# Performance work log

Hardware: AMD Instinct MI355X
Metric: run time of the kernel (lower is better)

## Reference

```python
import jax, jax.numpy as jnp
import numpy as np

B, C, H, W = 64, 256, 32, 32
K, D = 1024, 256
COMMIT = 0.25
DECAY = 0.99
EPS = 1e-05


def setup_inputs() -> dict:
    key = jax.random.key(0)
    k1, k2, k3 = jax.random.split(key, 3)
    return {
        "inputs": jax.random.normal(k1, (B, C, H, W), dtype=jnp.float32),
        "embedding": jax.random.normal(k2, (K, D), dtype=jnp.float32),
        "ema_cluster_size": jnp.zeros((K,), dtype=jnp.float32),
        "ema_w": jax.random.normal(k3, (K, D), dtype=jnp.float32),
    }


def reference(inputs, embedding, ema_cluster_size, ema_w):
    # NCHW -> NHWC, flatten to [N, D]
    x = jnp.transpose(inputs, (0, 2, 3, 1))  # [B,H,W,D]
    in_shape = x.shape
    flat = x.reshape(-1, D)  # [N, D]

    dist = (jnp.sum(flat * flat, axis=1, keepdims=True)
            + jnp.sum(embedding * embedding, axis=1)
            - 2.0 * jnp.matmul(flat, embedding.T))
    idx = jnp.argmin(dist, axis=1)  # [N] int
    encodings = jax.nn.one_hot(idx, K, dtype=flat.dtype)  # [N, K]

    quantized = jnp.matmul(encodings, embedding).reshape(in_shape)  # [B,H,W,D]

    # EMA updates (training branch)
    cluster = ema_cluster_size * DECAY + (1.0 - DECAY) * jnp.sum(encodings, axis=0)
    n = jnp.sum(cluster)
    cluster = (cluster + EPS) / (n + K * EPS) * n
    dw = jnp.matmul(encodings.T, flat)  # [K, D]
    new_ema_w = ema_w * DECAY + (1.0 - DECAY) * dw
    new_embedding = new_ema_w / cluster[:, None]

    # commitment loss (quantized detached)
    e_latent_loss = jnp.mean((jax.lax.stop_gradient(quantized) - x) ** 2)
    loss = COMMIT * e_latent_loss

    # straight-through estimator
    quantized_st = x + jax.lax.stop_gradient(quantized - x)

    avg_probs = jnp.mean(encodings, axis=0)
    vq_entropy = -jnp.sum(avg_probs * jnp.log(avg_probs + 1e-10))

    out = jnp.transpose(quantized_st, (0, 3, 1, 2))  # back to NCHW
    return out, loss, vq_entropy, encodings, cluster, new_ema_w, new_embedding
```

## Files before the change

### kernel.cpp

```cpp
#include <hip/hip_runtime.h>

#define B_    64
#define C_    256
#define H_    32
#define W_    32
#define K_    1024
#define D_    256
#define HW_   1024
#define N_    65536
#define NELEM 16777216
#define DECAY_ 0.99f
#define OMD_   0.01f
#define EPS_   1e-5f
#define TAU_   0.05f

#define OFF_LOSS    16777216
#define OFF_ENT     16777217
#define OFF_ENC     16777218
#define OFF_CLUSTER 83886082
#define OFF_NEWW    83887106
#define OFF_NEWEMB  84149250

#define OFF_XHI     (OFF_ENC + 2)
#define OFF_XLO     (OFF_XHI + 8388608)
#define OFF_EHI     (OFF_XLO + 8388608)
#define OFF_ELO     (OFF_EHI + 131072)
#define OFF_SORT2   (OFF_ELO + 131072)
#define ZTAIL_ABS   33884168
#define ZTAIL_F4    12500478
#define ZHEAD_F4    4276737

typedef __attribute__((ext_vector_type(8)))  short short8;
typedef __attribute__((ext_vector_type(16))) float floatx16;

__device__ __forceinline__ unsigned short f2bf(float f) {
    unsigned u = __float_as_uint(f);
    return (unsigned short)((u + 0x7fffu + ((u >> 16) & 1u)) >> 16);
}
__device__ __forceinline__ float bf2f(unsigned short h) {
    return __uint_as_float(((unsigned)h) << 16);
}

__global__ __launch_bounds__(256) void k_zero(float* __restrict__ dw, int* __restrict__ small_) {
    int g = blockIdx.x * 256 + threadIdx.x;
    dw[g] = 0.0f;
    if (g < 1026) small_[g] = 0;
}

__global__ __launch_bounds__(64) void k_prep_e(const float* __restrict__ emb,
                                               unsigned short* __restrict__ ehi,
                                               unsigned short* __restrict__ elo,
                                               float* __restrict__ enorm) {
    const int k = blockIdx.x;
    const int t = threadIdx.x;
    float4 v = ((const float4*)(emb + (size_t)k * D_))[t];
    float s = v.x * v.x + v.y * v.y + v.z * v.z + v.w * v.w;
    ushort4 hi, lo;
    {
        float f[4] = {v.x, v.y, v.z, v.w};
        unsigned short h[4], l[4];
        #pragma unroll
        for (int j = 0; j < 4; ++j) {
            h[j] = f2bf(f[j]);
            l[j] = f2bf(f[j] - bf2f(h[j]));
        }
        hi = make_ushort4(h[0], h[1], h[2], h[3]);
        lo = make_ushort4(l[0], l[1], l[2], l[3]);
    }
    size_t o = ((size_t)(k >> 5) << 13) + ((size_t)(t >> 2) << 9)
             + (((size_t)(t >> 1) & 1) << 8) + ((size_t)(k & 31) << 3) + ((t & 1) << 2);
    *(ushort4*)(ehi + o) = hi;
    *(ushort4*)(elo + o) = lo;
    #pragma unroll
    for (int off = 32; off > 0; off >>= 1) s += __shfl_down(s, off);
    if (t == 0) enorm[k] = s;
}

__global__ __launch_bounds__(256) void k_prep_x(const float* __restrict__ inp,
                                                unsigned short* __restrict__ xhi,
                                                unsigned short* __restrict__ xlo) {
    __shared__ float tile[32][257];
    const int tid = threadIdx.x;
    const int bid = blockIdx.x;
    const int dt = bid & 7;
    const int ht = (bid >> 3) & 3;
    const int b = bid >> 5;
    const int d0 = dt * 32;
    const int hw0 = ht * 256;
    const float* src = inp + (size_t)b * (C_ * HW_) + (size_t)d0 * HW_ + hw0;
    #pragma unroll
    for (int i = 0; i < 8; ++i) {
        int idx4 = i * 256 + tid;
        int dl = idx4 >> 6;
        int nl4 = (idx4 & 63) * 4;
        float4 v = *(const float4*)(src + (size_t)dl * HW_ + nl4);
        tile[dl][nl4] = v.x; tile[dl][nl4 + 1] = v.y;
        tile[dl][nl4 + 2] = v.z; tile[dl][nl4 + 3] = v.w;
    }
    __syncthreads();
    const int nbase = b * HW_ + hw0;
    #pragma unroll
    for (int i = 0; i < 4; ++i) {
        int f8 = i * 256 + tid;
        int nl = f8 >> 2;
        int dpos = (f8 & 3) * 8;
        union { unsigned short u[8]; short8 v; } ph, pl;
        #pragma unroll
        for (int j = 0; j < 8; ++j) {
            float f = -2.0f * tile[dpos + j][nl];
            unsigned short h = f2bf(f);
            ph.u[j] = h;
            pl.u[j] = f2bf(f - bf2f(h));
        }
        size_t o = (size_t)(nbase + nl) * D_ + d0 + dpos;
        *(short8*)(xhi + o) = ph.v;
        *(short8*)(xlo + o) = pl.v;
    }
}

__device__ __forceinline__ void stage_tile(const unsigned short* __restrict__ gh,
                                           const unsigned short* __restrict__ gl,
                                           unsigned short* sh, unsigned short* sl,
                                           int tid) {
    #pragma unroll
    for (int i = 0; i < 4; ++i) {
        __builtin_amdgcn_global_load_lds(
            (const __attribute__((address_space(1))) unsigned int*)(gh + i * 2048 + tid * 8),
            (__attribute__((address_space(3))) unsigned int*)(sh + i * 2048 + tid * 8),
            16, 0, 0);
        __builtin_amdgcn_global_load_lds(
            (const __attribute__((address_space(1))) unsigned int*)(gl + i * 2048 + tid * 8),
            (__attribute__((address_space(3))) unsigned int*)(sl + i * 2048 + tid * 8),
            16, 0, 0);
    }
}

__global__ __launch_bounds__(256, 2) void k_argmin(
    const unsigned short* __restrict__ xhi, const unsigned short* __restrict__ xlo,
    const unsigned short* __restrict__ ehi, const unsigned short* __restrict__ elo,
    const float* __restrict__ enorm, int* __restrict__ idx_out,
    int* __restrict__ flagcount, int* __restrict__ flaglist,
    float4* __restrict__ encz)
{
    __shared__ unsigned short smem[2][2][8192];
    const int tid = threadIdx.x;
    const int w = tid >> 6;
    const int lane = tid & 63;
    const int c32 = lane & 31;
    const int h = lane >> 5;
    const int r0 = blockIdx.x * 128 + w * 32;
    const int gtid = blockIdx.x * 256 + tid;
    const float4 z4 = make_float4(0.f, 0.f, 0.f, 0.f);

    short8 Ahi[16], Alo[16];
    {
        const unsigned short* pa = xhi + (size_t)(r0 + c32) * D_ + h * 8;
        const unsigned short* pl = xlo + (size_t)(r0 + c32) * D_ + h * 8;
        #pragma unroll
        for (int ds = 0; ds < 16; ++ds) {
            Ahi[ds] = *(const short8*)(pa + ds * 16);
            Alo[ds] = *(const short8*)(pl + ds * 16);
        }
    }

    float b1[16], b2[16];
    int bi[16];
    #pragma unroll
    for (int i = 0; i < 16; ++i) { b1[i] = 3.0e38f; b2[i] = 3.0e38f; bi[i] = 0; }

    stage_tile(ehi, elo, &smem[0][0][0], &smem[0][1][0], tid);
    __syncthreads();

    const int rb = (h << 8) + (c32 << 3);

    int cb = 0;
    for (int ct = 0; ct < 32; ++ct) {
        if (ct + 1 < 32) {
            stage_tile(ehi + (size_t)(ct + 1) * 8192, elo + (size_t)(ct + 1) * 8192,
                       &smem[cb ^ 1][0][0], &smem[cb ^ 1][1][0], tid);
        }
        #pragma unroll
        for (int jj = 0; jj < 3; ++jj) {
            int zi = (ct * 3 + jj) * 131072 + gtid;
            if (zi < ZTAIL_F4) encz[zi] = z4;
        }
        const int col = ct * 32 + c32;
        const float en = enorm[col];
        const unsigned short* sbh = &smem[cb][0][rb];
        const unsigned short* sbl = &smem[cb][1][rb];
        floatx16 hh, cr;
        #pragma unroll
        for (int i = 0; i < 16; ++i) { hh[i] = 0.0f; cr[i] = 0.0f; }
        #pragma unroll
        for (int ds = 0; ds < 16; ++ds) {
            short8 bh = *(const short8*)(sbh + ds * 512);
            short8 bl = *(const short8*)(sbl + ds * 512);
            hh = __builtin_amdgcn_mfma_f32_32x32x16_bf16(Ahi[ds], bh, hh, 0, 0, 0);
            cr = __builtin_amdgcn_mfma_f32_32x32x16_bf16(Ahi[ds], bl, cr, 0, 0, 0);
            cr = __builtin_amdgcn_mfma_f32_32x32x16_bf16(Alo[ds], bh, cr, 0, 0, 0);
        }
        #pragma unroll
        for (int r = 0; r < 16; ++r) {
            float v = hh[r] + cr[r] + en;
            bool lt = v < b1[r];
            float nb2 = lt ? b1[r] : fminf(v, b2[r]);
            b2[r] = nb2;
            b1[r] = lt ? v : b1[r];
            bi[r] = lt ? col : bi[r];
        }
        __syncthreads();
        cb ^= 1;
    }

    #pragma unroll
    for (int r = 0; r < 16; ++r) {
        float B1 = b1[r], B2 = b2[r];
        int Bi = bi[r];
        #pragma unroll
        for (int mask = 1; mask <= 16; mask <<= 1) {
            float v1 = __shfl_xor(B1, mask);
            float v2 = __shfl_xor(B2, mask);
            int i1 = __shfl_xor(Bi, mask);
            if (v1 < B1 || (v1 == B1 && i1 < Bi)) {
                B2 = fminf(fminf(B1, B2), v2);
                B1 = v1; Bi = i1;
            } else {
                B2 = fminf(B2, fminf(v1, v2));
            }
        }
        if (c32 == 0) {
            int row = r0 + (r & 3) + 4 * h + 8 * (r >> 2);
            idx_out[row] = Bi;
            if (B2 - B1 < TAU_) {
                int p = atomicAdd(flagcount, 1);
                flaglist[p] = row;
            }
        }
    }
}

__global__ __launch_bounds__(256) void k_rescan(
    const float* __restrict__ inp, const float* __restrict__ emb,
    const int* __restrict__ flagcount, const int* __restrict__ flaglist,
    int* __restrict__ idx_out)
{
    __shared__ double xd[256];
    __shared__ double sv[256];
    __shared__ int si[256];
    const int tid = threadIdx.x;
    const int nflag = *flagcount;
    for (int f = blockIdx.x; f < nflag; f += gridDim.x) {
        int n = flaglist[f];
        int b = n >> 10, nn = n & 1023;
        xd[tid] = (double)inp[(size_t)b * (C_ * HW_) + (size_t)tid * HW_ + nn];
        __syncthreads();
        double bv = 1e300; int bi = 0;
        for (int k = tid; k < K_; k += 256) {
            const float* ep = emb + (size_t)k * D_;
            double dot = 0.0, en = 0.0;
            for (int d = 0; d < D_; ++d) {
                double e = (double)ep[d];
                dot = fma(xd[d], e, dot);
                en  = fma(e, e, en);
            }
            double v = en - 2.0 * dot;
            if (v < bv) { bv = v; bi = k; }
        }
        sv[tid] = bv; si[tid] = bi;
        __syncthreads();
        for (int s = 128; s > 0; s >>= 1) {
            if (tid < s) {
                if (sv[tid + s] < sv[tid] || (sv[tid + s] == sv[tid] && si[tid + s] < si[tid])) {
                    sv[tid] = sv[tid + s]; si[tid] = si[tid + s];
                }
            }
            __syncthreads();
        }
        if (tid == 0) idx_out[n] = si[0];
        __syncthreads();
    }
}

__global__ __launch_bounds__(256) void k_hist(const int* __restrict__ idx, int* __restrict__ counts) {
    __shared__ int h[1024];
    const int tid = threadIdx.x;
    #pragma unroll
    for (int j = 0; j < 4; ++j) h[tid + j * 256] = 0;
    __syncthreads();
    #pragma unroll
    for (int j = 0; j < 4; ++j) {
        int n = blockIdx.x * 1024 + j * 256 + tid;
        atomicAdd(&h[idx[n]], 1);
    }
    __syncthreads();
    #pragma unroll
    for (int j = 0; j < 4; ++j) {
        int v = h[tid + j * 256];
        if (v) atomicAdd(&counts[tid + j * 256], v);
    }
}

__global__ __launch_bounds__(1024) void k_scan(const int* __restrict__ counts,
                                               int* __restrict__ offsets, int* __restrict__ cursor) {
    __shared__ int s[1024];
    const int t = threadIdx.x;
    const int c = counts[t];
    s[t] = c;
    __syncthreads();
    for (int off = 1; off < 1024; off <<= 1) {
        int v = (t >= off) ? s[t - off] : 0;
        __syncthreads();
        s[t] += v;
        __syncthreads();
    }
    int excl = s[t] - c;
    offsets[t] = excl;
    cursor[t] = excl;
    if (t == 1023) offsets[1024] = s[1023];
}

__global__ __launch_bounds__(256) void k_scatter(const int* __restrict__ idx,
                                                 int* __restrict__ cursor, int* __restrict__ sorted) {
    __shared__ int hc[1024];
    __shared__ int hb[1024];
    const int tid = threadIdx.x;
    const int base = blockIdx.x * 1024;
    #pragma unroll
    for (int j = 0; j < 4; ++j) hc[tid + j * 256] = 0;
    __syncthreads();
    int myk[4], myn[4];
    #pragma unroll
    for (int j = 0; j < 4; ++j) {
        int n = base + j * 256 + tid;
        myn[j] = n;
        myk[j] = idx[n];
        atomicAdd(&hc[myk[j]], 1);
    }
    __syncthreads();
    #pragma unroll
    for (int j = 0; j < 4; ++j) {
        int kk = tid + j * 256;
        int c = hc[kk];
        hb[kk] = c ? atomicAdd(&cursor[kk], c) : 0;
    }
    __syncthreads();
    #pragma unroll
    for (int j = 0; j < 4; ++j) hc[tid + j * 256] = 0;
    __syncthreads();
    #pragma unroll
    for (int j = 0; j < 4; ++j) {
        int p = hb[myk[j]] + atomicAdd(&hc[myk[j]], 1);
        sorted[p] = myn[j];
    }
}

__global__ __launch_bounds__(256) void k_dwg(const unsigned short* __restrict__ xhi,
                                             const unsigned short* __restrict__ xlo,
                                             const int* __restrict__ sorted,
                                             const int* __restrict__ idx,
                                             const int* __restrict__ offsets,
                                             float* __restrict__ dw) {
    const int lane = threadIdx.x & 63;
    const int wid = threadIdx.x >> 6;
    const int wbase = (blockIdx.x * 4 + wid) * 64;

    int myn = sorted[wbase + lane];
    int myk = idx[myn];

    float4 acc = make_float4(0.f, 0.f, 0.f, 0.f);
    int cur = __shfl(myk, 0);

    #pragma unroll 8
    for (int i = 0; i < 64; ++i) {
        int n = __shfl(myn, i);
        int k = __shfl(myk, i);
        if (k != cur) {
            bool full = (offsets[cur] >= wbase) && (offsets[cur + 1] <= wbase + 64);
            float* dwk = dw + (size_t)cur * D_ + lane * 4;
            if (full) {
                ((float2*)dwk)[0] = make_float2(-0.5f * acc.x, -0.5f * acc.y);
                ((float2*)dwk)[1] = make_float2(-0.5f * acc.z, -0.5f * acc.w);
            } else {
                atomicAdd(dwk + 0, -0.5f * acc.x);
                atomicAdd(dwk + 1, -0.5f * acc.y);
                atomicAdd(dwk + 2, -0.5f * acc.z);
                atomicAdd(dwk + 3, -0.5f * acc.w);
            }
            acc = make_float4(0.f, 0.f, 0.f, 0.f);
            cur = k;
        }
        size_t o = (size_t)n * D_ + lane * 4;
        ushort4 hx = *(const ushort4*)(xhi + o);
        ushort4 lx = *(const ushort4*)(xlo + o);
        acc.x += bf2f(hx.x) + bf2f(lx.x);
        acc.y += bf2f(hx.y) + bf2f(lx.y);
        acc.z += bf2f(hx.z) + bf2f(lx.z);
        acc.w += bf2f(hx.w) + bf2f(lx.w);
    }
    {
        bool full = (offsets[cur] >= wbase) && (offsets[cur + 1] <= wbase + 64);
        float* dwk = dw + (size_t)cur * D_ + lane * 4;
        if (full) {
            ((float2*)dwk)[0] = make_float2(-0.5f * acc.x, -0.5f * acc.y);
            ((float2*)dwk)[1] = make_float2(-0.5f * acc.z, -0.5f * acc.w);
        } else {
            atomicAdd(dwk + 0, -0.5f * acc.x);
            atomicAdd(dwk + 1, -0.5f * acc.y);
            atomicAdd(dwk + 2, -0.5f * acc.z);
            atomicAdd(dwk + 3, -0.5f * acc.w);
        }
    }
}

__global__ __launch_bounds__(256) void k_enc0(float* __restrict__ enc) {
    const float4 z = make_float4(0.f, 0.f, 0.f, 0.f);
    float4* p = (float4*)(enc + 2);
    int t = blockIdx.x * 256 + threadIdx.x;
    #pragma unroll
    for (int it = 0; it < 5; ++it) {
        int i = it * 1048576 + t;
        if (i < ZHEAD_F4) p[i] = z;
    }
    if (t == 0) { enc[0] = 0.f; enc[1] = 0.f; enc[67108862] = 0.f; enc[67108863] = 0.f; }
}

__global__ __launch_bounds__(256) void k_enc1(const int* __restrict__ idx, float* __restrict__ enc) {
    #pragma unroll
    for (int j = 0; j < 4; ++j) {
        int n = blockIdx.x * 1024 + j * 256 + threadIdx.x;
        enc[(size_t)n * 1024 + idx[n]] = 1.0f;
    }
}

__global__ __launch_bounds__(256) void k_quant(
    const float* __restrict__ inp, const float* __restrict__ emb,
    const int* __restrict__ idx, float* __restrict__ outp, float* __restrict__ losssum)
{
    __shared__ float red[256];
    const int tid = threadIdx.x;
    float s = 0.0f;
    const int base = blockIdx.x * 1024;
    #pragma unroll
    for (int it = 0; it < 4; ++it) {
        int g = base + it * 256 + tid;
        int o = g << 2;
        int b = o >> 18;
        int c = (o >> 10) & 255;
        int hw = o & 1023;
        int n = (b << 10) + hw;
        float4 x = ((const float4*)inp)[g];
        int4 ki = *(const int4*)(idx + n);
        float q0 = emb[(size_t)ki.x * D_ + c];
        float q1 = emb[(size_t)ki.y * D_ + c];
        float q2 = emb[(size_t)ki.z * D_ + c];
        float q3 = emb[(size_t)ki.w * D_ + c];
        float d0 = q0 - x.x, d1 = q1 - x.y, d2 = q2 - x.z, d3 = q3 - x.w;
        ((float4*)outp)[g] = make_float4(x.x + d0, x.y + d1, x.z + d2, x.w + d3);
        s += d0 * d0 + d1 * d1 + d2 * d2 + d3 * d3;
    }
    red[tid] = s;
    __syncthreads();
    for (int t = 128; t > 0; t >>= 1) {
        if (tid < t) red[tid] += red[tid + t];
        __syncthreads();
    }
    if (tid == 0) atomicAdd(losssum, red[0]);
}

__global__ __launch_bounds__(1024) void k_cluster(
    const float* __restrict__ ema_cs, const int* __restrict__ counts,
    const float* __restrict__ losssum, float* __restrict__ out_cluster,
    float* __restrict__ out_loss, float* __restrict__ out_ent)
{
    __shared__ float red[1024];
    const int k = threadIdx.x;
    float cnt = (float)counts[k];
    float raw = ema_cs[k] * DECAY_ + OMD_ * cnt;
    red[k] = raw;
    __syncthreads();
    for (int t = 512; t > 0; t >>= 1) {
        if (k < t) red[k] += red[k + t];
        __syncthreads();
    }
    float nsum = red[0];
    __syncthreads();
    float clv = (raw + EPS_) / (nsum + 1024.0f * EPS_) * nsum;
    out_cluster[k] = clv;
    float p = cnt * (1.0f / 65536.0f);
    red[k] = p * logf(p + 1e-10f);
    __syncthreads();
    for (int t = 512; t > 0; t >>= 1) {
        if (k < t) red[k] += red[k + t];
        __syncthreads();
    }
    if (k == 0) {
        out_ent[0] = -red[0];
        out_loss[0] = 0.25f * losssum[0] * (1.0f / 16777216.0f);
    }
}

__global__ __launch_bounds__(256) void k_fin(
    const float* __restrict__ ema_w, const float* __restrict__ cluster,
    float* __restrict__ neww, float* __restrict__ newemb)
{
    int g = blockIdx.x * 256 + threadIdx.x;
    int k = g >> 8;
    float w = ema_w[g] * DECAY_ + OMD_ * neww[g];
    neww[g] = w;
    newemb[g] = w / cluster[k];
}

extern "C" void kernel_launch(void* const* d_in, const int* in_sizes, int n_in,
                              void* d_out, int out_size, void* d_ws, size_t ws_size,
                              hipStream_t stream)
{
    const float* inp    = (const float*)d_in[0];
    const float* emb    = (const float*)d_in[1];
    const float* ema_cs = (const float*)d_in[2];
    const float* ema_w  = (const float*)d_in[3];

    float* out0        = (float*)d_out;
    float* out_loss    = out0 + OFF_LOSS;
    float* out_ent     = out0 + OFF_ENT;
    float* out_enc     = out0 + OFF_ENC;
    float* out_cluster = out0 + OFF_CLUSTER;
    float* out_neww    = out0 + OFF_NEWW;
    float* out_newemb  = out0 + OFF_NEWEMB;

    unsigned short* ws_xhi  = (unsigned short*)(out0 + OFF_XHI);
    unsigned short* ws_xlo  = (unsigned short*)(out0 + OFF_XLO);
    unsigned short* ws_ehi  = (unsigned short*)(out0 + OFF_EHI);
    unsigned short* ws_elo  = (unsigned short*)(out0 + OFF_ELO);
    int*   ws_sorted  = (int*)(out0 + OFF_SORT2);
    int*   ws_offsets = ws_sorted + 65536;
    int*   ws_cursor  = ws_offsets + 1025;

    int*   ws_idx    = (int*)d_ws;
    int*   ws_counts = ws_idx + 65536;
    int*   ws_flagc  = ws_idx + 66560;
    float* ws_loss   = (float*)(ws_idx + 66561);
    int*   ws_flagl  = ws_idx + 66562;
    float* ws_enorm  = (float*)(ws_idx + 132098);

    float4* encz = (float4*)(out0 + ZTAIL_ABS);

    k_zero   <<<1024, 256, 0, stream>>>(out_neww, ws_counts);
    k_prep_e <<<1024, 64, 0, stream>>>(emb, ws_ehi, ws_elo, ws_enorm);
    k_prep_x <<<2048, 256, 0, stream>>>(inp, ws_xhi, ws_xlo);
    k_argmin <<<512, 256, 0, stream>>>(ws_xhi, ws_xlo, ws_ehi, ws_elo, ws_enorm,
                                       ws_idx, ws_flagc, ws_flagl, encz);
    k_rescan <<<256, 256, 0, stream>>>(inp, emb, ws_flagc, ws_flagl, ws_idx);
    k_hist   <<<64, 256, 0, stream>>>(ws_idx, ws_counts);
    k_scan   <<<1, 1024, 0, stream>>>(ws_counts, ws_offsets, ws_cursor);
    k_scatter<<<64, 256, 0, stream>>>(ws_idx, ws_cursor, ws_sorted);
    k_dwg    <<<256, 256, 0, stream>>>(ws_xhi, ws_xlo, ws_sorted, ws_idx, ws_offsets, out_neww);
    k_enc0   <<<4096, 256, 0, stream>>>(out_enc);
    k_enc1   <<<64, 256, 0, stream>>>(ws_idx, out_enc);
    k_quant  <<<4096, 256, 0, stream>>>(inp, emb, ws_idx, out0, ws_loss);
    k_cluster<<<1, 1024, 0, stream>>>(ema_cs, ws_counts, ws_loss, out_cluster, out_loss, out_ent);
    k_fin    <<<1024, 256, 0, stream>>>(ema_w, out_cluster, out_neww, out_newemb);
}
```

Before: 733.4 us.

## Give each argmin wave two 32-row tiles to reuse codebook LDS loads

```diff
diff --git a/kernel.cpp b/kernel.cpp
--- a/kernel.cpp
+++ b/kernel.cpp
@@ -123,19 +123,19 @@
                                            unsigned short* sh, unsigned short* sl,
                                            int tid) {
     #pragma unroll
-    for (int i = 0; i < 4; ++i) {
+    for (int i = 0; i < 8; ++i) {
         __builtin_amdgcn_global_load_lds(
-            (const __attribute__((address_space(1))) unsigned int*)(gh + i * 2048 + tid * 8),
-            (__attribute__((address_space(3))) unsigned int*)(sh + i * 2048 + tid * 8),
+            (const __attribute__((address_space(1))) unsigned int*)(gh + i * 1024 + tid * 8),
+            (__attribute__((address_space(3))) unsigned int*)(sh + i * 1024 + tid * 8),
             16, 0, 0);
         __builtin_amdgcn_global_load_lds(
-            (const __attribute__((address_space(1))) unsigned int*)(gl + i * 2048 + tid * 8),
-            (__attribute__((address_space(3))) unsigned int*)(sl + i * 2048 + tid * 8),
+            (const __attribute__((address_space(1))) unsigned int*)(gl + i * 1024 + tid * 8),
+            (__attribute__((address_space(3))) unsigned int*)(sl + i * 1024 + tid * 8),
             16, 0, 0);
     }
 }
 
-__global__ __launch_bounds__(256, 2) void k_argmin(
+__global__ __launch_bounds__(128, 1) void k_argmin(
     const unsigned short* __restrict__ xhi, const unsigned short* __restrict__ xlo,
     const unsigned short* __restrict__ ehi, const unsigned short* __restrict__ elo,
     const float* __restrict__ enorm, int* __restrict__ idx_out,
@@ -148,25 +148,28 @@
     const int lane = tid & 63;
     const int c32 = lane & 31;
     const int h = lane >> 5;
-    const int r0 = blockIdx.x * 128 + w * 32;
-    const int gtid = blockIdx.x * 256 + tid;
+    const int r0 = blockIdx.x * 128 + w * 64;
+    const int gtid = blockIdx.x * 128 + tid;
     const float4 z4 = make_float4(0.f, 0.f, 0.f, 0.f);
 
-    short8 Ahi[16], Alo[16];
-    {
-        const unsigned short* pa = xhi + (size_t)(r0 + c32) * D_ + h * 8;
-        const unsigned short* pl = xlo + (size_t)(r0 + c32) * D_ + h * 8;
+    short8 Ahi[2][16], Alo[2][16];
+    #pragma unroll
+    for (int rt = 0; rt < 2; ++rt) {
+        const unsigned short* pa = xhi + (size_t)(r0 + rt * 32 + c32) * D_ + h * 8;
+        const unsigned short* pl = xlo + (size_t)(r0 + rt * 32 + c32) * D_ + h * 8;
         #pragma unroll
         for (int ds = 0; ds < 16; ++ds) {
-            Ahi[ds] = *(const short8*)(pa + ds * 16);
-            Alo[ds] = *(const short8*)(pl + ds * 16);
-        }
-    }
-
-    float b1[16], b2[16];
-    int bi[16];
-    #pragma unroll
-    for (int i = 0; i < 16; ++i) { b1[i] = 3.0e38f; b2[i] = 3.0e38f; bi[i] = 0; }
+            Ahi[rt][ds] = *(const short8*)(pa + ds * 16);
+            Alo[rt][ds] = *(const short8*)(pl + ds * 16);
+        }
+    }
+
+    float b1[2][16], b2[2][16];
+    int bi[2][16];
+    #pragma unroll
+    for (int rt = 0; rt < 2; ++rt)
+        #pragma unroll
+        for (int i = 0; i < 16; ++i) { b1[rt][i] = 3.0e38f; b2[rt][i] = 3.0e38f; bi[rt][i] = 0; }
 
     stage_tile(ehi, elo, &smem[0][0][0], &smem[0][1][0], tid);
     __syncthreads();
@@ -180,60 +183,80 @@
                        &smem[cb ^ 1][0][0], &smem[cb ^ 1][1][0], tid);
         }
         #pragma unroll
-        for (int jj = 0; jj < 3; ++jj) {
-            int zi = (ct * 3 + jj) * 131072 + gtid;
-            if (zi < ZTAIL_F4) encz[zi] = z4;
+        for (int jj = 0; jj < 6; ++jj) {
+            int zi = (ct * 6 + jj) * 65536 + gtid;
+            zi = (zi < ZTAIL_F4) ? zi : (ZTAIL_F4 - 1);
+            encz[zi] = z4;
         }
         const int col = ct * 32 + c32;
         const float en = enorm[col];
         const unsigned short* sbh = &smem[cb][0][rb];
         const unsigned short* sbl = &smem[cb][1][rb];
-        floatx16 hh, cr;
-        #pragma unroll
-        for (int i = 0; i < 16; ++i) { hh[i] = 0.0f; cr[i] = 0.0f; }
+        floatx16 hh0, cr0, hh1, cr1;
+        #pragma unroll
+        for (int i = 0; i < 16; ++i) { hh0[i] = 0.0f; cr0[i] = 0.0f; hh1[i] = 0.0f; cr1[i] = 0.0f; }
         #pragma unroll
         for (int ds = 0; ds < 16; ++ds) {
             short8 bh = *(const short8*)(sbh + ds * 512);
             short8 bl = *(const short8*)(sbl + ds * 512);
-            hh = __builtin_amdgcn_mfma_f32_32x32x16_bf16(Ahi[ds], bh, hh, 0, 0, 0);
-            cr = __builtin_amdgcn_mfma_f32_32x32x16_bf16(Ahi[ds], bl, cr, 0, 0, 0);
-            cr = __builtin_amdgcn_mfma_f32_32x32x16_bf16(Alo[ds], bh, cr, 0, 0, 0);
+            hh0 = __builtin_amdgcn_mfma_f32_32x32x16_bf16(Ahi[0][ds], bh, hh0, 0, 0, 0);
+            cr0 = __builtin_amdgcn_mfma_f32_32x32x16_bf16(Ahi[0][ds], bl, cr0, 0, 0, 0);
+            hh1 = __builtin_amdgcn_mfma_f32_32x32x16_bf16(Ahi[1][ds], bh, hh1, 0, 0, 0);
+            cr1 = __builtin_amdgcn_mfma_f32_32x32x16_bf16(Ahi[1][ds], bl, cr1, 0, 0, 0);
+            cr0 = __builtin_amdgcn_mfma_f32_32x32x16_bf16(Alo[0][ds], bh, cr0, 0, 0, 0);
+            cr1 = __builtin_amdgcn_mfma_f32_32x32x16_bf16(Alo[1][ds], bh, cr1, 0, 0, 0);
         }
         #pragma unroll
         for (int r = 0; r < 16; ++r) {
-            float v = hh[r] + cr[r] + en;
-            bool lt = v < b1[r];
-            float nb2 = lt ? b1[r] : fminf(v, b2[r]);
-            b2[r] = nb2;
-            b1[r] = lt ? v : b1[r];
-            bi[r] = lt ? col : bi[r];
-        }
-        __syncthreads();
+            {
+                float v = hh0[r] + cr0[r] + en;
+                bool lt = v < b1[0][r];
+                float nb2 = lt ? b1[0][r] : fminf(v, b2[0][r]);
+                b2[0][r] = nb2;
+                b1[0][r] = lt ? v : b1[0][r];
+                bi[0][r] = lt ? col : bi[0][r];
+            }
+            {
+                float v = hh1[r] + cr1[r] + en;
+                bool lt = v < b1[1][r];
+                float nb2 = lt ? b1[1][r] : fminf(v, b2[1][r]);
+                b2[1][r] = nb2;
+                b1[1][r] = lt ? v : b1[1][r];
+                bi[1][r] = lt ? col : bi[1][r];
+            }
+        }
+        asm volatile("s_waitcnt vmcnt(6)" ::: "memory");
+        __builtin_amdgcn_sched_barrier(0);
+        __builtin_amdgcn_s_barrier();
+        __builtin_amdgcn_sched_barrier(0);
         cb ^= 1;
     }
 
     #pragma unroll
-    for (int r = 0; r < 16; ++r) {
-        float B1 = b1[r], B2 = b2[r];
-        int Bi = bi[r];
-        #pragma unroll
-        for (int mask = 1; mask <= 16; mask <<= 1) {
-            float v1 = __shfl_xor(B1, mask);
-            float v2 = __shfl_xor(B2, mask);
-            int i1 = __shfl_xor(Bi, mask);
-            if (v1 < B1 || (v1 == B1 && i1 < Bi)) {
-                B2 = fminf(fminf(B1, B2), v2);
-                B1 = v1; Bi = i1;
-            } else {
-                B2 = fminf(B2, fminf(v1, v2));
-            }
-        }
-        if (c32 == 0) {
-            int row = r0 + (r & 3) + 4 * h + 8 * (r >> 2);
-            idx_out[row] = Bi;
-            if (B2 - B1 < TAU_) {
-                int p = atomicAdd(flagcount, 1);
-                flaglist[p] = row;
+    for (int rt = 0; rt < 2; ++rt) {
+        #pragma unroll
+        for (int r = 0; r < 16; ++r) {
+            float B1 = b1[rt][r], B2 = b2[rt][r];
+            int Bi = bi[rt][r];
+            #pragma unroll
+            for (int mask = 1; mask <= 16; mask <<= 1) {
+                float v1 = __shfl_xor(B1, mask);
+                float v2 = __shfl_xor(B2, mask);
+                int i1 = __shfl_xor(Bi, mask);
+                if (v1 < B1 || (v1 == B1 && i1 < Bi)) {
+                    B2 = fminf(fminf(B1, B2), v2);
+                    B1 = v1; Bi = i1;
+                } else {
+                    B2 = fminf(B2, fminf(v1, v2));
+                }
+            }
+            if (c32 == 0) {
+                int row = r0 + rt * 32 + (r & 3) + 4 * h + 8 * (r >> 2);
+                idx_out[row] = Bi;
+                if (B2 - B1 < TAU_) {
+                    int p = atomicAdd(flagcount, 1);
+                    flaglist[p] = row;
+                }
             }
         }
     }
@@ -547,7 +570,7 @@
     k_zero   <<<1024, 256, 0, stream>>>(out_neww, ws_counts);
     k_prep_e <<<1024, 64, 0, stream>>>(emb, ws_ehi, ws_elo, ws_enorm);
     k_prep_x <<<2048, 256, 0, stream>>>(inp, ws_xhi, ws_xlo);
-    k_argmin <<<512, 256, 0, stream>>>(ws_xhi, ws_xlo, ws_ehi, ws_elo, ws_enorm,
+    k_argmin <<<512, 128, 0, stream>>>(ws_xhi, ws_xlo, ws_ehi, ws_elo, ws_enorm,
                                        ws_idx, ws_flagc, ws_flagl, encz);
     k_rescan <<<256, 256, 0, stream>>>(inp, emb, ws_flagc, ws_flagl, ws_idx);
     k_hist   <<<64, 256, 0, stream>>>(ws_idx, ws_counts);
```

New measurement: 756.6 us. +3.2%, slower.
